# Kernel tuning notes

Measured on AMD Instinct MI355X. Metric: run time of the kernel, lower is better.

Reference implementation:

```python
import jax, jax.numpy as jnp
import numpy as np

# Ordered bi-bi mechanism, species order per _build_species_list:
# [E, EA, EQ, EAB, A, B, P, Q] -> indices 0..7
# Transitions: E+A<->EA, EA+B<->EAB, EAB<->EQ+P, EQ<->E+Q (all reversible)
N_SPECIES = 8
N_TRANS = 4

# forward: rate * [enzyme] * prod([substrates]); -1 = no factor (padded)
ENZ_F = np.array([0, 1, 3, 2], dtype=np.int32)          # E, EA, EAB, EQ
SUB_F = np.array([[4], [5], [-1], [-1]], dtype=np.int32)  # A, B, -, -
# reverse: rate * [to-enzyme] * prod([products])
ENZ_R = np.array([1, 3, 2, 0], dtype=np.int32)          # EA, EAB, EQ, E
PROD_R = np.array([[-1], [-1], [6], [7]], dtype=np.int32)  # -, -, P, Q
REV_MASK = np.array([1.0, 1.0, 1.0, 1.0], dtype=np.float32)

# Stoichiometry (n_trans, n_species), applied as dydt += v_net[:,None]*S[i]
S_FORWARD = np.array([
    [-1,  1,  0,  0, -1,  0,  0,  0],
    [ 0, -1,  0,  1,  0, -1,  0,  0],
    [ 0,  0,  1, -1,  0,  0,  1,  0],
    [ 1,  0, -1,  0,  0,  0,  0,  1],
], dtype=np.float32)


def _masked_gather_prod(y, idx):
    # y: (B, n_species); idx: (n_trans, k) with -1 padding
    safe = jnp.maximum(idx, 0)
    g = y[:, safe.reshape(-1)].reshape(y.shape[0], idx.shape[0], idx.shape[1])  # (B,T,k)
    g = jnp.where(idx[None, :, :] >= 0, g, 1.0)
    return jnp.prod(g, axis=-1)  # (B, T)


def setup_inputs() -> dict:
    key = jax.random.key(0)
    k1, k2, k3 = jax.random.split(key, 3)
    B = 2_000_000
    return {
        "t": jnp.zeros((1,), dtype=jnp.float32),
        "y": jax.random.uniform(k1, (B, N_SPECIES), dtype=jnp.float32),
        "forward_rates": jax.random.uniform(k2, (B, N_TRANS), dtype=jnp.float32),
        "reverse_rates": jax.random.uniform(k3, (B, N_TRANS), dtype=jnp.float32),
    }


def reference(t, y, forward_rates, reverse_rates):
    enz_f = jnp.asarray(ENZ_F)
    enz_r = jnp.asarray(ENZ_R)
    sub_f = jnp.asarray(SUB_F)
    prod_r = jnp.asarray(PROD_R)
    S = jnp.asarray(S_FORWARD)
    rev_mask = jnp.asarray(REV_MASK)

    # v_forward[b,i] = k_f[b,i] * y[b, enz_f[i]] * prod_j y[b, sub_f[i,j]]
    v_f = forward_rates * y[:, enz_f] * _masked_gather_prod(y, sub_f)
    # v_reverse analogous, zeroed for irreversible transitions
    v_r = reverse_rates * y[:, enz_r] * _masked_gather_prod(y, prod_r) * rev_mask[None, :]
    v_net = v_f - v_r  # (B, T)
    # dydt[b,s] = sum_i v_net[b,i] * S[i,s]
    return jnp.einsum("bt,ts->bs", v_net, S)
```

## Files before the change

### kernel.cpp

```cpp
#include <hip/hip_runtime.h>


__global__ __launch_bounds__(256) void ode_kernel(
    const float4* __restrict__ y4,
    const float4* __restrict__ kf4,
    const float4* __restrict__ kr4,
    float4* __restrict__ out4,
    int n2)
{
    int t = blockIdx.x * blockDim.x + threadIdx.x;
    if (t >= n2) return;

    int e = t >> 1;
    int h = t & 1;

    float4 q = y4[t];

    float4 p;
    p.x = __shfl_xor(q.x, 1);
    p.y = __shfl_xor(q.y, 1);
    p.z = __shfl_xor(q.z, 1);
    p.w = __shfl_xor(q.w, 1);

    float4 ya = h ? p : q;
    float4 yb = h ? q : p;

    const float4* __restrict__ rp = h ? kr4 : kf4;
    float4 mine = rp[e];
    float4 other;
    other.x = __shfl_xor(mine.x, 1);
    other.y = __shfl_xor(mine.y, 1);
    other.z = __shfl_xor(mine.z, 1);
    other.w = __shfl_xor(mine.w, 1);

    float4 f = h ? other : mine;
    float4 r = h ? mine : other;

    float E  = ya.x, EA = ya.y, EQ = ya.z, EAB = ya.w;
    float A  = yb.x, Bc = yb.y, P  = yb.z, Q   = yb.w;

    float v0 = f.x * E   * A  - r.x * EA;
    float v1 = f.y * EA  * Bc - r.y * EAB;
    float v2 = f.z * EAB      - r.z * EQ * P;
    float v3 = f.w * EQ       - r.w * E  * Q;

    float4 o;
    if (h == 0) {
        o.x = v3 - v0;
        o.y = v0 - v1;
        o.z = v2 - v3;
        o.w = v1 - v2;
    } else {
        o.x = -v0;
        o.y = -v1;
        o.z =  v2;
        o.w =  v3;
    }

    out4[t] = o;
}

extern "C" void kernel_launch(void* const* d_in, const int* in_sizes, int n_in,
                              void* d_out, int out_size, void* d_ws, size_t ws_size,
                              hipStream_t stream) {
    const float4* y4  = (const float4*)d_in[1];
    const float4* kf4 = (const float4*)d_in[2];
    const float4* kr4 = (const float4*)d_in[3];
    float4* out4 = (float4*)d_out;
    int B  = in_sizes[1] / 8;
    int n2 = 2 * B;

    int block = 256;
    int grid = (n2 + block - 1) / block;
    ode_kernel<<<grid, block, 0, stream>>>(y4, kf4, kr4, out4, n2);
}
```

Measured before the change: 168.2 us.

## Use grid-stride loop with load prefetch and nontemporal output stores

The launch becomes a grid-stride loop capped at 2048 blocks. Each thread loads the next row's state and rate vectors before computing and storing the current row, so load latency overlaps with compute. Output is written with nontemporal stores to avoid polluting cache with streaming data. The risk is that the capped grid occupies the GPU less fully than one thread per element would, and the extra live registers for the prefetch may reduce occupancy.

```diff
diff --git a/kernel.cpp b/kernel.cpp
--- a/kernel.cpp
+++ b/kernel.cpp
@@ -1,21 +1,9 @@
 #include <hip/hip_runtime.h>
 
 
-__global__ __launch_bounds__(256) void ode_kernel(
-    const float4* __restrict__ y4,
-    const float4* __restrict__ kf4,
-    const float4* __restrict__ kr4,
-    float4* __restrict__ out4,
-    int n2)
-{
-    int t = blockIdx.x * blockDim.x + threadIdx.x;
-    if (t >= n2) return;
+typedef float nfloat4 __attribute__((ext_vector_type(4)));
 
-    int e = t >> 1;
-    int h = t & 1;
-
-    float4 q = y4[t];
-
+__device__ __forceinline__ nfloat4 process_row(float4 q, float4 mine, int h) {
     float4 p;
     p.x = __shfl_xor(q.x, 1);
     p.y = __shfl_xor(q.y, 1);
@@ -25,8 +13,6 @@
     float4 ya = h ? p : q;
     float4 yb = h ? q : p;
 
-    const float4* __restrict__ rp = h ? kr4 : kf4;
-    float4 mine = rp[e];
     float4 other;
     other.x = __shfl_xor(mine.x, 1);
     other.y = __shfl_xor(mine.y, 1);
@@ -44,7 +30,7 @@
     float v2 = f.z * EAB      - r.z * EQ * P;
     float v3 = f.w * EQ       - r.w * E  * Q;
 
-    float4 o;
+    nfloat4 o;
     if (h == 0) {
         o.x = v3 - v0;
         o.y = v0 - v1;
@@ -56,8 +42,39 @@
         o.z =  v2;
         o.w =  v3;
     }
+    return o;
+}
 
-    out4[t] = o;
+__global__ __launch_bounds__(256) void ode_kernel(
+    const float4* __restrict__ y4,
+    const float4* __restrict__ kf4,
+    const float4* __restrict__ kr4,
+    nfloat4* __restrict__ out4,
+    int n2)
+{
+    const int t = blockIdx.x * 256 + threadIdx.x;
+    const int S = gridDim.x * 256;
+    const int h = t & 1;
+    const float4* __restrict__ rp = h ? kr4 : kf4;
+
+    int r = t;
+    if (r >= n2) return;
+
+    float4 q = y4[r];
+    float4 m = rp[r >> 1];
+
+    for (int rn = r + S; rn < n2; rn += S) {
+        float4 qn = y4[rn];
+        float4 mn = rp[rn >> 1];
+
+        nfloat4 o = process_row(q, m, h);
+        __builtin_nontemporal_store(o, &out4[r]);
+
+        q = qn; m = mn; r = rn;
+    }
+
+    nfloat4 o = process_row(q, m, h);
+    __builtin_nontemporal_store(o, &out4[r]);
 }
 
 extern "C" void kernel_launch(void* const* d_in, const int* in_sizes, int n_in,
@@ -66,11 +83,12 @@
     const float4* y4  = (const float4*)d_in[1];
     const float4* kf4 = (const float4*)d_in[2];
     const float4* kr4 = (const float4*)d_in[3];
-    float4* out4 = (float4*)d_out;
+    nfloat4* out4 = (nfloat4*)d_out;
     int B  = in_sizes[1] / 8;
     int n2 = 2 * B;
 
     int block = 256;
-    int grid = (n2 + block - 1) / block;
+    int full  = (n2 + block - 1) / block;
+    int grid  = full < 2048 ? full : 2048;
     ode_kernel<<<grid, block, 0, stream>>>(y4, kf4, kr4, out4, n2);
 }
```

Result: slower. 173.4 us (+3.1%).
